# Kernel tuning notes

Hardware: AMD Instinct MI355X
Metric: run time of the kernel (lower is better)

## Reference

```python
import jax, jax.numpy as jnp
import numpy as np

N_NODES = 100000
N_EDGES = 1600000
D_IN = 256
D_OUT = 128


def _gcn_norm(edge_index, num_nodes):
    # Add self-loops and compute symmetric normalization D^-1/2 A D^-1/2 (PyG GCNConv default).
    src, dst = edge_index[0], edge_index[1]
    loop = jnp.arange(num_nodes, dtype=edge_index.dtype)
    src = jnp.concatenate([src, loop])
    dst = jnp.concatenate([dst, loop])
    deg = jax.ops.segment_sum(jnp.ones_like(dst, dtype=jnp.float32), dst, num_segments=num_nodes)
    dinv = jnp.where(deg > 0, jax.lax.rsqrt(jnp.maximum(deg, 1.0)), 0.0)
    norm = dinv[src] * dinv[dst]  # [E + N]
    return src, dst, norm


def _gcn_conv(x, W, b, src, dst, norm, num_nodes):
    h = x @ W  # [N, d_out] transform first (d_out <= d_in keeps message traffic low)
    msg = h[src] * norm[:, None]  # [E+N, d_out] gather + scale
    out = jax.ops.segment_sum(msg, dst, num_segments=num_nodes)  # scatter-add
    return out + b


def setup_inputs() -> dict:
    key = jax.random.key(0)
    ks = jax.random.split(key, 8)
    x = jax.random.normal(ks[0], (N_NODES, D_IN), dtype=jnp.float32)
    edge_index = jax.random.randint(ks[1], (2, N_EDGES), 0, N_NODES, dtype=jnp.int64)
    s = 0.05
    return {
        "x": x,
        "edge_index": edge_index,
        "W1": jax.random.normal(ks[2], (D_IN, D_OUT), dtype=jnp.float32) * s,
        "b1": jnp.zeros((D_OUT,), dtype=jnp.float32),
        "W_mu": jax.random.normal(ks[3], (D_OUT, D_OUT), dtype=jnp.float32) * s,
        "b_mu": jnp.zeros((D_OUT,), dtype=jnp.float32),
        "W_ls": jax.random.normal(ks[4], (D_OUT, D_OUT), dtype=jnp.float32) * s,
        "b_ls": jnp.zeros((D_OUT,), dtype=jnp.float32),
    }


def reference(x, edge_index, W1, b1, W_mu, b_mu, W_ls, b_ls):
    num_nodes = x.shape[0]
    src, dst, norm = _gcn_norm(edge_index, num_nodes)
    h = jax.nn.relu(_gcn_conv(x, W1, b1, src, dst, norm, num_nodes))
    mu = _gcn_conv(h, W_mu, b_mu, src, dst, norm, num_nodes)
    logstd = _gcn_conv(h, W_ls, b_ls, src, dst, norm, num_nodes)
    return (mu, logstd)
```

## Files before the change

### kernel.cpp

```cpp
#include <hip/hip_runtime.h>
#include <hip/hip_bf16.h>
#include <hip/hip_fp16.h>

typedef __attribute__((ext_vector_type(8))) short short8;
typedef __attribute__((ext_vector_type(8))) _Float16 f16x8;
typedef __attribute__((ext_vector_type(4))) float f32x4;


#define EPB 16384

__global__ __launch_bounds__(256) void k_lhist(const int* __restrict__ dst, int* __restrict__ histT,
                                               int nE, int nblk, int nbins) {
  __shared__ int c[1024];
  int tid = threadIdx.x;
  for (int i = tid; i < nbins; i += 256) c[i] = 0;
  __syncthreads();
  int blk = blockIdx.x;
  int e0 = blk * EPB;
  int e1 = min(nE, e0 + EPB);
  if (e1 - e0 == EPB) {
#pragma unroll
    for (int it = 0; it < EPB / 1024; ++it) {
      int4 d = *(const int4*)(dst + e0 + it * 1024 + tid * 4);
      atomicAdd(&c[d.x >> 7], 1);
      atomicAdd(&c[d.y >> 7], 1);
      atomicAdd(&c[d.z >> 7], 1);
      atomicAdd(&c[d.w >> 7], 1);
    }
  } else {
    for (int i = e0 + tid; i < e1; i += 256) atomicAdd(&c[dst[i] >> 7], 1);
  }
  __syncthreads();
  for (int i = tid; i < nbins; i += 256) histT[i * nblk + blk] = c[i];
}

__global__ __launch_bounds__(256) void k_lscatter(
    const int* __restrict__ src, const int* __restrict__ dst, const int* __restrict__ subPtr,
    int* __restrict__ binned, int nE, int nblk, int nbins) {
  __shared__ int cur[1024];
  int tid = threadIdx.x;
  int blk = blockIdx.x;
  for (int i = tid; i < nbins; i += 256) cur[i] = subPtr[i * nblk + blk];
  __syncthreads();
  int e0 = blk * EPB;
  int e1 = min(nE, e0 + EPB);
  if (e1 - e0 == EPB) {
#pragma unroll
    for (int it = 0; it < EPB / 1024; ++it) {
      int base = e0 + it * 1024 + tid * 4;
      int4 s = *(const int4*)(src + base);
      int4 d = *(const int4*)(dst + base);
      int p0 = atomicAdd(&cur[d.x >> 7], 1);
      int p1 = atomicAdd(&cur[d.y >> 7], 1);
      int p2 = atomicAdd(&cur[d.z >> 7], 1);
      int p3 = atomicAdd(&cur[d.w >> 7], 1);
      binned[p0] = s.x | ((d.x & 127) << 20);
      binned[p1] = s.y | ((d.y & 127) << 20);
      binned[p2] = s.z | ((d.z & 127) << 20);
      binned[p3] = s.w | ((d.w & 127) << 20);
    }
  } else {
    for (int i = e0 + tid; i < e1; i += 256) {
      int d = dst[i];
      int pos = atomicAdd(&cur[d >> 7], 1);
      binned[pos] = src[i] | ((d & 127) << 20);
    }
  }
}

__global__ __launch_bounds__(256) void k_bin_cnt(
    const int* __restrict__ binned, const int* __restrict__ subPtr,
    int* __restrict__ cnt, int nE, int nblk, int nbins, int n) {
  __shared__ int c128[128];
  int b = blockIdx.x;
  int tid = threadIdx.x;
  if (tid < 128) c128[tid] = 0;
  __syncthreads();
  int s0 = subPtr[b * nblk];
  int s1 = (b + 1 < nbins) ? subPtr[(b + 1) * nblk] : nE;
  for (int i = s0 + tid; i < s1; i += 256)
    atomicAdd(&c128[(binned[i] >> 20) & 127], 1);
  __syncthreads();
  if (tid < 128) {
    int idx = (b << 7) + tid;
    if (idx < n) cnt[idx] = c128[tid];
  }
}

__global__ __launch_bounds__(256) void k_bin_place(
    const int* __restrict__ binned, const int* __restrict__ subPtr,
    const int* __restrict__ rowptr, int* __restrict__ col, int nE, int nblk, int nbins, int n) {
  __shared__ int cur128[128];
  int b = blockIdx.x;
  int tid = threadIdx.x;
  if (tid < 128) {
    int idx = (b << 7) + tid;
    cur128[tid] = (idx < n) ? rowptr[idx] : 0;
  }
  __syncthreads();
  int s0 = subPtr[b * nblk];
  int s1 = (b + 1 < nbins) ? subPtr[(b + 1) * nblk] : nE;
  for (int i = s0 + tid; i < s1; i += 256) {
    int e = binned[i];
    int pos = atomicAdd(&cur128[(e >> 20) & 127], 1);
    col[pos] = e & 0xFFFFF;
  }
}


__global__ void k_blocksum(const int* __restrict__ cnt, int* __restrict__ bsum, int n) {
  __shared__ int red[256];
  int tid = threadIdx.x;
  int base = blockIdx.x * 1024 + tid * 4;
  int s = 0;
#pragma unroll
  for (int i = 0; i < 4; i++) { int idx = base + i; if (idx < n) s += cnt[idx]; }
  red[tid] = s;
  __syncthreads();
  for (int off = 128; off > 0; off >>= 1) {
    if (tid < off) red[tid] += red[tid + off];
    __syncthreads();
  }
  if (tid == 0) bsum[blockIdx.x] = red[0];
}

__global__ void k_scan_bsum(int* __restrict__ bsum, int nb) {
  __shared__ int s[128];
  int tid = threadIdx.x;
  int v = (tid < nb) ? bsum[tid] : 0;
  s[tid] = v;
  __syncthreads();
  for (int off = 1; off < 128; off <<= 1) {
    int t = (tid >= off) ? s[tid - off] : 0;
    __syncthreads();
    s[tid] += t;
    __syncthreads();
  }
  if (tid < nb) bsum[tid] = s[tid] - v;
}

__global__ void k_scan_final(const int* __restrict__ cnt, const int* __restrict__ bsum,
                             int* __restrict__ rowptr, float* __restrict__ dinv, int n) {
  __shared__ int tsum[256];
  int tid = threadIdx.x;
  int base = blockIdx.x * 1024 + tid * 4;
  int v[4]; int s = 0;
#pragma unroll
  for (int i = 0; i < 4; i++) { v[i] = (base + i < n) ? cnt[base + i] : 0; s += v[i]; }
  tsum[tid] = s;
  __syncthreads();
  for (int off = 1; off < 256; off <<= 1) {
    int t = (tid >= off) ? tsum[tid - off] : 0;
    __syncthreads();
    tsum[tid] += t;
    __syncthreads();
  }
  int run = bsum[blockIdx.x] + tsum[tid] - s;
#pragma unroll
  for (int i = 0; i < 4; i++) {
    int idx = base + i;
    if (idx < n) {
      rowptr[idx] = run;
      if (dinv) dinv[idx] = rsqrtf((float)(v[i] + 1));
      run += v[i];
    }
  }
}


__global__ void k_prep_w(const float* __restrict__ W1,
                         const float* __restrict__ Wmu, const float* __restrict__ Wls,
                         const float* __restrict__ bmu, const float* __restrict__ bls,
                         __half* __restrict__ W1T, __half* __restrict__ WcT,
                         float* __restrict__ bcat) {
  int i = blockIdx.x * blockDim.x + threadIdx.x;
  if (i < 128 * 256) {
    int n = i >> 8, k = i & 255;
    W1T[i] = __float2half(W1[k * 128 + n]);
  } else if (i < 2 * 128 * 256) {
    int j = i - 128 * 256;
    int n = j >> 7, k = j & 127;
    float f = (n < 128) ? Wmu[k * 128 + n] : Wls[k * 128 + (n - 128)];
    WcT[j] = __float2half(f);
  } else if (i < 2 * 128 * 256 + 256) {
    int n = i - 2 * 128 * 256;
    bcat[n] = (n < 128) ? bmu[n] : bls[n - 128];
  }
}


#define LP 40

template <int AFMT, int OFMT>
__global__ __launch_bounds__(256) void k_gemm_mfma(
    const void* __restrict__ Av, const __half* __restrict__ WT,
    const float* __restrict__ bias, void* __restrict__ out0, void* __restrict__ out1,
    int M, int K, int split_out) {
  __shared__ _Float16 As[128 * LP];
  __shared__ _Float16 Bs[128 * LP];

  const int tid = threadIdx.x;
  const int lane = tid & 63;
  const int wv = tid >> 6;
  const int wr = wv >> 1, wc = wv & 1;
  const int rsel = lane >> 4;
  const int rrow = lane & 15;
  const int row0 = blockIdx.x * 128;
  const int col0 = blockIdx.y * 128;

  f32x4 acc[4][4];
#pragma unroll
  for (int m = 0; m < 4; m++)
#pragma unroll
    for (int n = 0; n < 4; n++) acc[m][n] = (f32x4){0.f, 0.f, 0.f, 0.f};

  const int srow = tid >> 1;
  const int skh = (tid & 1) * 16;

  for (int k0 = 0; k0 < K; k0 += 32) {
    if (row0 + srow < M) {
      if (AFMT == 0) {
        const float* src = (const float*)Av + (size_t)(row0 + srow) * K + k0 + skh;
        float4 f0 = *(const float4*)(src);
        float4 f1 = *(const float4*)(src + 4);
        float4 f2 = *(const float4*)(src + 8);
        float4 f3 = *(const float4*)(src + 12);
        f16x8 v0, v1;
        v0[0]=(_Float16)f0.x; v0[1]=(_Float16)f0.y; v0[2]=(_Float16)f0.z; v0[3]=(_Float16)f0.w;
        v0[4]=(_Float16)f1.x; v0[5]=(_Float16)f1.y; v0[6]=(_Float16)f1.z; v0[7]=(_Float16)f1.w;
        v1[0]=(_Float16)f2.x; v1[1]=(_Float16)f2.y; v1[2]=(_Float16)f2.z; v1[3]=(_Float16)f2.w;
        v1[4]=(_Float16)f3.x; v1[5]=(_Float16)f3.y; v1[6]=(_Float16)f3.z; v1[7]=(_Float16)f3.w;
        *(f16x8*)&As[srow * LP + skh]     = v0;
        *(f16x8*)&As[srow * LP + skh + 8] = v1;
      } else {
        const _Float16* src = (const _Float16*)Av + (size_t)(row0 + srow) * K + k0 + skh;
        *(f16x8*)&As[srow * LP + skh]     = *(const f16x8*)src;
        *(f16x8*)&As[srow * LP + skh + 8] = *(const f16x8*)(src + 8);
      }
    } else {
      f16x8 z = (f16x8){0,0,0,0,0,0,0,0};
      *(f16x8*)&As[srow * LP + skh] = z; *(f16x8*)&As[srow * LP + skh + 8] = z;
    }
    {
      const _Float16* s = (const _Float16*)WT + (size_t)(col0 + srow) * K + k0 + skh;
      *(f16x8*)&Bs[srow * LP + skh]     = *(const f16x8*)s;
      *(f16x8*)&Bs[srow * LP + skh + 8] = *(const f16x8*)(s + 8);
    }
    __syncthreads();

    f16x8 fa[4], fb[4];
#pragma unroll
    for (int m = 0; m < 4; m++)
      fa[m] = *(f16x8*)&As[(wr * 64 + m * 16 + rrow) * LP + rsel * 8];
#pragma unroll
    for (int n = 0; n < 4; n++)
      fb[n] = *(f16x8*)&Bs[(wc * 64 + n * 16 + rrow) * LP + rsel * 8];
#pragma unroll
    for (int m = 0; m < 4; m++)
#pragma unroll
      for (int n = 0; n < 4; n++)
        acc[m][n] = __builtin_amdgcn_mfma_f32_16x16x32_f16(fa[m], fb[n], acc[m][n], 0, 0, 0);
    __syncthreads();
  }

#pragma unroll
  for (int n = 0; n < 4; n++) {
    int col = col0 + wc * 64 + n * 16 + rrow;
    float badd = bias ? bias[col] : 0.f;
    void* dstBase = out0;
    int c = col;
    if (split_out && c >= 128) { dstBase = out1; c -= 128; }
#pragma unroll
    for (int m = 0; m < 4; m++) {
      f32x4 v = acc[m][n];
#pragma unroll
      for (int r = 0; r < 4; r++) {
        int row = row0 + wr * 64 + m * 16 + rsel * 4 + r;
        if (row < M) {
          if (OFMT == 0)
            ((float*)dstBase)[(size_t)row * 128 + c] = v[r] + badd;
          else
            ((__half*)dstBase)[(size_t)row * 128 + c] = __float2half(v[r] + badd);
        }
      }
    }
  }
}


__global__ __launch_bounds__(256) void k_spmm_h(
    const __half* __restrict__ in, const int* __restrict__ rowptr,
    const int* __restrict__ cnt, const int* __restrict__ col,
    const float* __restrict__ dinv,
    const float* __restrict__ bias, __half* __restrict__ out,
    int n, int use_bias, int relu_out) {
  int node = blockIdx.x * 4 + (threadIdx.x >> 6);
  if (node >= n) return;
  int lane = threadIdx.x & 63;

  const __half2* inp = (const __half2*)in;
  float di = dinv[node];
  float2 v = __half22float2(inp[(size_t)node * 64 + lane]);
  float accx = di * v.x;
  float accy = di * v.y;

  int beg = rowptr[node];
  int m = cnt[node];
  int i = 0;
  for (; i + 8 <= m; i += 8) {
    int c[8];
#pragma unroll
    for (int j = 0; j < 8; j++) c[j] = col[beg + i + j];
    float e[8];
#pragma unroll
    for (int j = 0; j < 8; j++) e[j] = dinv[c[j]];
    float2 u[8];
#pragma unroll
    for (int j = 0; j < 8; j++) u[j] = __half22float2(inp[(size_t)c[j] * 64 + lane]);
#pragma unroll
    for (int j = 0; j < 8; j++) { accx += e[j] * u[j].x; accy += e[j] * u[j].y; }
  }
  if (i < m) {
    int c[8];
#pragma unroll
    for (int j = 0; j < 8; j++) c[j] = col[(i + j < m) ? (beg + i + j) : beg];
    float e[8];
#pragma unroll
    for (int j = 0; j < 8; j++) e[j] = (i + j < m) ? dinv[c[j]] : 0.f;
    float2 u[8];
#pragma unroll
    for (int j = 0; j < 8; j++) u[j] = __half22float2(inp[(size_t)c[j] * 64 + lane]);
#pragma unroll
    for (int j = 0; j < 8; j++) { accx += e[j] * u[j].x; accy += e[j] * u[j].y; }
  }
  accx *= di;
  accy *= di;
  if (use_bias) {
    accx += bias[2 * lane];
    accy += bias[2 * lane + 1];
  }
  if (relu_out) {
    accx = fmaxf(accx, 0.f);
    accy = fmaxf(accy, 0.f);
  }
  ((__half2*)(out + (size_t)node * 128))[lane] = __floats2half2_rn(accx, accy);
}


extern "C" void kernel_launch(void* const* d_in, const int* in_sizes, int n_in,
                              void* d_out, int out_size, void* d_ws, size_t ws_size,
                              hipStream_t stream) {
  const float* x   = (const float*)d_in[0];
  const int*   ei  = (const int*)d_in[1];
  const float* W1  = (const float*)d_in[2];
  const float* b1  = (const float*)d_in[3];
  const float* Wmu = (const float*)d_in[4];
  const float* bmu = (const float*)d_in[5];
  const float* Wls = (const float*)d_in[6];
  const float* bls = (const float*)d_in[7];

  int N = in_sizes[0] / 256;
  int E = in_sizes[1] / 2;
  const int* src = ei;
  const int* dst = ei + E;

  int NBINS = (N + 127) >> 7;
  int NBLK  = (E + EPB - 1) / EPB;
  int NS    = NBINS * NBLK;

  char* ws = (char*)d_ws;
  size_t o = 0;
  auto alloc = [&](size_t b) { size_t c = o; o = (o + b + 511) & ~(size_t)511; return c; };
  int*   cnt     = (int*)(ws + alloc((size_t)N * 4));
  int*   rowptr  = (int*)(ws + alloc((size_t)N * 4));
  float* dinv    = (float*)(ws + alloc((size_t)N * 4));
  int*   bsum    = (int*)(ws + alloc(512));
  int*   histT   = (int*)(ws + alloc((size_t)NS * 4));
  int*   subPtr  = (int*)(ws + alloc((size_t)NS * 4));
  int*   col     = (int*)(ws + alloc((size_t)E * 4));
  int*   binned  = (int*)(ws + alloc((size_t)E * 4));
  __half* W1T  = (__half*)(ws + alloc(128 * 256 * 2));
  __half* WcT  = (__half*)(ws + alloc(256 * 128 * 2));
  float*  bcat = (float*)(ws + alloc(256 * 4));
  __half* h0   = (__half*)(ws + alloc((size_t)N * 128 * 2));
  __half* hBuf = (__half*)(ws + alloc((size_t)N * 128 * 2));

  float* outMu = (float*)d_out;
  float* outLs = outMu + (size_t)N * 128;

  int nbScanN = (N + 1023) / 1024;
  int nbScanS = (NS + 1023) / 1024;

  k_lhist<<<NBLK, 256, 0, stream>>>(dst, histT, E, NBLK, NBINS);
  k_blocksum<<<nbScanS, 256, 0, stream>>>(histT, bsum, NS);
  k_scan_bsum<<<1, 128, 0, stream>>>(bsum, nbScanS);
  k_scan_final<<<nbScanS, 256, 0, stream>>>(histT, bsum, subPtr, nullptr, NS);
  k_lscatter<<<NBLK, 256, 0, stream>>>(src, dst, subPtr, binned, E, NBLK, NBINS);
  k_bin_cnt<<<NBINS, 256, 0, stream>>>(binned, subPtr, cnt, E, NBLK, NBINS, N);
  k_blocksum<<<nbScanN, 256, 0, stream>>>(cnt, bsum, N);
  k_scan_bsum<<<1, 128, 0, stream>>>(bsum, nbScanN);
  k_scan_final<<<nbScanN, 256, 0, stream>>>(cnt, bsum, rowptr, dinv, N);
  k_bin_place<<<NBINS, 256, 0, stream>>>(binned, subPtr, rowptr, col, E, NBLK, NBINS, N);

  k_prep_w<<<(2 * 128 * 256 + 256 + 255) / 256, 256, 0, stream>>>(
      W1, Wmu, Wls, bmu, bls, W1T, WcT, bcat);

  int gx = (N + 127) / 128;
  k_gemm_mfma<0, 1><<<dim3(gx, 1), 256, 0, stream>>>(x, W1T, nullptr, h0, nullptr, N, 256, 0);
  k_spmm_h<<<(N + 3) / 4, 256, 0, stream>>>(h0, rowptr, cnt, col, dinv, b1, hBuf, N, 1, 1);
  k_spmm_h<<<(N + 3) / 4, 256, 0, stream>>>(hBuf, rowptr, cnt, col, dinv, nullptr, h0, N, 0, 0);
  k_gemm_mfma<1, 0><<<dim3(gx, 2), 256, 0, stream>>>(h0, WcT, bcat, outMu, outLs, N, 128, 1);
}
```

Measured before the change: 306.9 us.

## Rewrite GEMMs to stream A directly from global with whole-B XOR-swizzled LDS tile

Replaces the LDS-staged, k-looped 128x128 MFMA GEMM with a kernel that loads the entire weight tile for its 128 output columns into shared memory once, using an XOR swizzle to avoid bank conflicts. A fragments are read straight from global memory into registers, with no A staging and no per-k-step barriers. Each block now covers 64 rows, each wave handling 16 rows by 128 columns. This removes the repeated syncthreads and A-tile LDS traffic, at the cost of 64KB of LDS per block for K=256, which may limit occupancy, and global A loads that are less coalesced.

```diff
diff --git a/kernel.cpp b/kernel.cpp
--- a/kernel.cpp
+++ b/kernel.cpp
@@ -5,7 +5,6 @@
 typedef __attribute__((ext_vector_type(8))) short short8;
 typedef __attribute__((ext_vector_type(8))) _Float16 f16x8;
 typedef __attribute__((ext_vector_type(4))) float f32x4;
-
 
 #define EPB 16384
 
@@ -189,99 +188,79 @@
 }
 
 
-#define LP 40
-
-template <int AFMT, int OFMT>
-__global__ __launch_bounds__(256) void k_gemm_mfma(
+template <int K, int AFMT, int OFMT>
+__global__ __launch_bounds__(256) void k_gemm_direct(
     const void* __restrict__ Av, const __half* __restrict__ WT,
     const float* __restrict__ bias, void* __restrict__ out0, void* __restrict__ out1,
-    int M, int K, int split_out) {
-  __shared__ _Float16 As[128 * LP];
-  __shared__ _Float16 Bs[128 * LP];
+    int M, int split_out) {
+  constexpr int C8 = K / 8;
+  __shared__ _Float16 Bs[128 * K];
 
   const int tid = threadIdx.x;
   const int lane = tid & 63;
-  const int wv = tid >> 6;
-  const int wr = wv >> 1, wc = wv & 1;
-  const int rsel = lane >> 4;
-  const int rrow = lane & 15;
-  const int row0 = blockIdx.x * 128;
+  const int w = tid >> 6;
+  const int lr = lane & 15;
+  const int lk = lane >> 4;
+  const int row0 = blockIdx.x * 64;
   const int col0 = blockIdx.y * 128;
 
-  f32x4 acc[4][4];
-#pragma unroll
-  for (int m = 0; m < 4; m++)
-#pragma unroll
-    for (int n = 0; n < 4; n++) acc[m][n] = (f32x4){0.f, 0.f, 0.f, 0.f};
-
-  const int srow = tid >> 1;
-  const int skh = (tid & 1) * 16;
-
-  for (int k0 = 0; k0 < K; k0 += 32) {
-    if (row0 + srow < M) {
+  {
+    const f16x8* gsrc = (const f16x8*)(WT + (size_t)col0 * K);
+    for (int i = tid; i < 128 * C8; i += 256) {
+      int n = i / C8, c = i % C8;
+      *(f16x8*)&Bs[n * K + ((c ^ (n & 7)) << 3)] = gsrc[i];
+    }
+  }
+  __syncthreads();
+
+  f32x4 acc[8];
+#pragma unroll
+  for (int n = 0; n < 8; n++) acc[n] = (f32x4){0.f, 0.f, 0.f, 0.f};
+
+  const int mrow = row0 + w * 16 + lr;
+  const bool valid = mrow < M;
+
+#pragma unroll
+  for (int ks = 0; ks < K / 32; ks++) {
+    f16x8 a;
+    if (valid) {
       if (AFMT == 0) {
-        const float* src = (const float*)Av + (size_t)(row0 + srow) * K + k0 + skh;
-        float4 f0 = *(const float4*)(src);
-        float4 f1 = *(const float4*)(src + 4);
-        float4 f2 = *(const float4*)(src + 8);
-        float4 f3 = *(const float4*)(src + 12);
-        f16x8 v0, v1;
-        v0[0]=(_Float16)f0.x; v0[1]=(_Float16)f0.y; v0[2]=(_Float16)f0.z; v0[3]=(_Float16)f0.w;
-        v0[4]=(_Float16)f1.x; v0[5]=(_Float16)f1.y; v0[6]=(_Float16)f1.z; v0[7]=(_Float16)f1.w;
-        v1[0]=(_Float16)f2.x; v1[1]=(_Float16)f2.y; v1[2]=(_Float16)f2.z; v1[3]=(_Float16)f2.w;
-        v1[4]=(_Float16)f3.x; v1[5]=(_Float16)f3.y; v1[6]=(_Float16)f3.z; v1[7]=(_Float16)f3.w;
-        *(f16x8*)&As[srow * LP + skh]     = v0;
-        *(f16x8*)&As[srow * LP + skh + 8] = v1;
+        const float* ap = (const float*)Av + (size_t)mrow * K + ks * 32 + lk * 8;
+        float4 f0 = *(const float4*)ap;
+        float4 f1 = *(const float4*)(ap + 4);
+        a[0] = (_Float16)f0.x; a[1] = (_Float16)f0.y; a[2] = (_Float16)f0.z; a[3] = (_Float16)f0.w;
+        a[4] = (_Float16)f1.x; a[5] = (_Float16)f1.y; a[6] = (_Float16)f1.z; a[7] = (_Float16)f1.w;
       } else {
-        const _Float16* src = (const _Float16*)Av + (size_t)(row0 + srow) * K + k0 + skh;
-        *(f16x8*)&As[srow * LP + skh]     = *(const f16x8*)src;
-        *(f16x8*)&As[srow * LP + skh + 8] = *(const f16x8*)(src + 8);
+        a = *(const f16x8*)((const _Float16*)Av + (size_t)mrow * K + ks * 32 + lk * 8);
       }
     } else {
-      f16x8 z = (f16x8){0,0,0,0,0,0,0,0};
-      *(f16x8*)&As[srow * LP + skh] = z; *(f16x8*)&As[srow * LP + skh + 8] = z;
-    }
-    {
-      const _Float16* s = (const _Float16*)WT + (size_t)(col0 + srow) * K + k0 + skh;
-      *(f16x8*)&Bs[srow * LP + skh]     = *(const f16x8*)s;
-      *(f16x8*)&Bs[srow * LP + skh + 8] = *(const f16x8*)(s + 8);
-    }
-    __syncthreads();
-
-    f16x8 fa[4], fb[4];
-#pragma unroll
-    for (int m = 0; m < 4; m++)
-      fa[m] = *(f16x8*)&As[(wr * 64 + m * 16 + rrow) * LP + rsel * 8];
-#pragma unroll
-    for (int n = 0; n < 4; n++)
-      fb[n] = *(f16x8*)&Bs[(wc * 64 + n * 16 + rrow) * LP + rsel * 8];
-#pragma unroll
-    for (int m = 0; m < 4; m++)
-#pragma unroll
-      for (int n = 0; n < 4; n++)
-        acc[m][n] = __builtin_amdgcn_mfma_f32_16x16x32_f16(fa[m], fb[n], acc[m][n], 0, 0, 0);
-    __syncthreads();
-  }
-
-#pragma unroll
-  for (int n = 0; n < 4; n++) {
-    int col = col0 + wc * 64 + n * 16 + rrow;
+      a = (f16x8){0, 0, 0, 0, 0, 0, 0, 0};
+    }
+#pragma unroll
+    for (int n = 0; n < 8; n++) {
+      int brow = n * 16 + lr;
+      int cr = ks * 4 + lk;
+      f16x8 b = *(const f16x8*)&Bs[brow * K + ((cr ^ (brow & 7)) << 3)];
+      acc[n] = __builtin_amdgcn_mfma_f32_16x16x32_f16(a, b, acc[n], 0, 0, 0);
+    }
+  }
+
+#pragma unroll
+  for (int n = 0; n < 8; n++) {
+    int col = col0 + n * 16 + lr;
     float badd = bias ? bias[col] : 0.f;
     void* dstBase = out0;
     int c = col;
     if (split_out && c >= 128) { dstBase = out1; c -= 128; }
-#pragma unroll
-    for (int m = 0; m < 4; m++) {
-      f32x4 v = acc[m][n];
-#pragma unroll
-      for (int r = 0; r < 4; r++) {
-        int row = row0 + wr * 64 + m * 16 + rsel * 4 + r;
-        if (row < M) {
-          if (OFMT == 0)
-            ((float*)dstBase)[(size_t)row * 128 + c] = v[r] + badd;
-          else
-            ((__half*)dstBase)[(size_t)row * 128 + c] = __float2half(v[r] + badd);
-        }
+    f32x4 v = acc[n];
+#pragma unroll
+    for (int r = 0; r < 4; r++) {
+      int row = row0 + w * 16 + lk * 4 + r;
+      if (row < M) {
+        if (OFMT == 0)
+          ((float*)dstBase)[(size_t)row * 128 + c] = v[r] + badd;
+        else
+          ((__half*)dstBase)[(size_t)row * 128 + c] = __float2half(v[r] + badd);
       }
     }
   }
@@ -405,9 +384,9 @@
   k_prep_w<<<(2 * 128 * 256 + 256 + 255) / 256, 256, 0, stream>>>(
       W1, Wmu, Wls, bmu, bls, W1T, WcT, bcat);
 
-  int gx = (N + 127) / 128;
-  k_gemm_mfma<0, 1><<<dim3(gx, 1), 256, 0, stream>>>(x, W1T, nullptr, h0, nullptr, N, 256, 0);
+  int gx = (N + 63) / 64;
+  k_gemm_direct<256, 0, 1><<<dim3(gx, 1), 256, 0, stream>>>(x, W1T, nullptr, h0, nullptr, N, 0);
   k_spmm_h<<<(N + 3) / 4, 256, 0, stream>>>(h0, rowptr, cnt, col, dinv, b1, hBuf, N, 1, 1);
   k_spmm_h<<<(N + 3) / 4, 256, 0, stream>>>(hBuf, rowptr, cnt, col, dinv, nullptr, h0, N, 0, 0);
-  k_gemm_mfma<1, 0><<<dim3(gx, 2), 256, 0, stream>>>(h0, WcT, bcat, outMu, outLs, N, 128, 1);
-}
+  k_gemm_direct<128, 1, 0><<<dim3(gx, 2), 256, 0, stream>>>(h0, WcT, bcat, outMu, outLs, N, 1);
+}
```

After: 309.3 us. About the same (+0.8%).

## Fuse second-layer SpMM aggregation with mu/logstd MFMA GEMM

Applied to the files above, without the earlier changes.

Replaces the separate second SpMM kernel and final GEMM with one kernel. Each block aggregates 16 nodes into a swizzled fp16 LDS tile, then runs 16x16x32 MFMAs against the concatenated mu/logstd weights and writes both outputs with bias. This removes the round trip of the intermediate aggregated features through global memory and one launch. In exchange, each wave handles 4 nodes serially, which may lower memory-level parallelism in the gather, and the weight matrix is reloaded from global memory by every block.

```diff
diff --git a/kernel.cpp b/kernel.cpp
--- a/kernel.cpp
+++ b/kernel.cpp
@@ -5,7 +5,6 @@
 typedef __attribute__((ext_vector_type(8))) short short8;
 typedef __attribute__((ext_vector_type(8))) _Float16 f16x8;
 typedef __attribute__((ext_vector_type(4))) float f32x4;
-
 
 #define EPB 16384
 
@@ -347,6 +346,95 @@
 }
 
 
+__global__ __launch_bounds__(256) void k_spmm_gemm(
+    const __half* __restrict__ in, const int* __restrict__ rowptr,
+    const int* __restrict__ cnt, const int* __restrict__ col,
+    const float* __restrict__ dinv,
+    const __half* __restrict__ WcT, const float* __restrict__ bcat,
+    float* __restrict__ out0, float* __restrict__ out1, int n) {
+  __shared__ _Float16 gt[16 * 128];
+  const int tid = threadIdx.x;
+  const int lane = tid & 63;
+  const int w = tid >> 6;
+  const __half2* inp = (const __half2*)in;
+
+  for (int q = 0; q < 4; q++) {
+    int li = w * 4 + q;
+    int node = blockIdx.x * 16 + li;
+    float accx = 0.f, accy = 0.f;
+    if (node < n) {
+      float di = dinv[node];
+      float2 v = __half22float2(inp[(size_t)node * 64 + lane]);
+      accx = di * v.x;
+      accy = di * v.y;
+      int beg = rowptr[node];
+      int m = cnt[node];
+      int i = 0;
+      for (; i + 8 <= m; i += 8) {
+        int c[8];
+#pragma unroll
+        for (int j = 0; j < 8; j++) c[j] = col[beg + i + j];
+        float e[8];
+#pragma unroll
+        for (int j = 0; j < 8; j++) e[j] = dinv[c[j]];
+        float2 u[8];
+#pragma unroll
+        for (int j = 0; j < 8; j++) u[j] = __half22float2(inp[(size_t)c[j] * 64 + lane]);
+#pragma unroll
+        for (int j = 0; j < 8; j++) { accx += e[j] * u[j].x; accy += e[j] * u[j].y; }
+      }
+      if (i < m) {
+        int c[8];
+#pragma unroll
+        for (int j = 0; j < 8; j++) c[j] = col[(i + j < m) ? (beg + i + j) : beg];
+        float e[8];
+#pragma unroll
+        for (int j = 0; j < 8; j++) e[j] = (i + j < m) ? dinv[c[j]] : 0.f;
+        float2 u[8];
+#pragma unroll
+        for (int j = 0; j < 8; j++) u[j] = __half22float2(inp[(size_t)c[j] * 64 + lane]);
+#pragma unroll
+        for (int j = 0; j < 8; j++) { accx += e[j] * u[j].x; accy += e[j] * u[j].y; }
+      }
+      accx *= di;
+      accy *= di;
+    }
+    int slot = (lane >> 2) ^ (li & 7);
+    *(__half2*)((char*)gt + li * 256 + slot * 16 + (lane & 3) * 4) =
+        __floats2half2_rn(accx, accy);
+  }
+  __syncthreads();
+
+  const int lr = lane & 15;
+  const int lk = lane >> 4;
+  f16x8 a[4];
+#pragma unroll
+  for (int ks = 0; ks < 4; ks++) {
+    int slot = (ks * 4 + lk) ^ (lr & 7);
+    a[ks] = *(const f16x8*)((const char*)gt + lr * 256 + slot * 16);
+  }
+#pragma unroll
+  for (int ct = 0; ct < 4; ct++) {
+    int colg = (w * 4 + ct) * 16 + lr;
+    f32x4 acc = (f32x4){0.f, 0.f, 0.f, 0.f};
+#pragma unroll
+    for (int ks = 0; ks < 4; ks++) {
+      f16x8 b = *(const f16x8*)((const _Float16*)WcT + (size_t)colg * 128 + ks * 32 + lk * 8);
+      acc = __builtin_amdgcn_mfma_f32_16x16x32_f16(a[ks], b, acc, 0, 0, 0);
+    }
+    float badd = bcat[colg];
+    float* dst = out0;
+    int c = colg;
+    if (c >= 128) { dst = out1; c -= 128; }
+#pragma unroll
+    for (int r = 0; r < 4; r++) {
+      int node = blockIdx.x * 16 + lk * 4 + r;
+      if (node < n) dst[(size_t)node * 128 + c] = acc[r] + badd;
+    }
+  }
+}
+
+
 extern "C" void kernel_launch(void* const* d_in, const int* in_sizes, int n_in,
                               void* d_out, int out_size, void* d_ws, size_t ws_size,
                               hipStream_t stream) {
@@ -408,6 +496,6 @@
   int gx = (N + 127) / 128;
   k_gemm_mfma<0, 1><<<dim3(gx, 1), 256, 0, stream>>>(x, W1T, nullptr, h0, nullptr, N, 256, 0);
   k_spmm_h<<<(N + 3) / 4, 256, 0, stream>>>(h0, rowptr, cnt, col, dinv, b1, hBuf, N, 1, 1);
-  k_spmm_h<<<(N + 3) / 4, 256, 0, stream>>>(hBuf, rowptr, cnt, col, dinv, nullptr, h0, N, 0, 0);
-  k_gemm_mfma<1, 0><<<dim3(gx, 2), 256, 0, stream>>>(h0, WcT, bcat, outMu, outLs, N, 128, 1);
-}
+  k_spmm_gemm<<<(N + 15) / 16, 256, 0, stream>>>(
+      hBuf, rowptr, cnt, col, dinv, WcT, bcat, outMu, outLs, N);
+}
```

After: 308.9 us. Within noise of the previous version (+0.6%).
